# Kernel tuning notes

Measured on AMD Instinct MI355X. Metric: run time of the kernel, lower is better.

## Reference

```python
import math
import jax, jax.numpy as jnp
import numpy as np

HIDDEN = 2048
N_HEAD = 32
N_KV = 8
HEAD_DIM = HIDDEN // N_HEAD  # 64
B, S = 2, 2048


def setup_inputs() -> dict:
    key = jax.random.key(0)
    ks = jax.random.split(key, 9)
    sc_h = 1.0 / math.sqrt(HIDDEN)
    return {
        "X": jax.random.normal(ks[0], (B, S, HIDDEN), jnp.float32),
        "Wq": jax.random.normal(ks[1], (HIDDEN, HIDDEN), jnp.float32) * sc_h,
        "bq": jax.random.normal(ks[2], (HIDDEN,), jnp.float32) * 0.01,
        "Wk": jax.random.normal(ks[3], (N_KV * HEAD_DIM, HIDDEN), jnp.float32) * sc_h,
        "bk": jax.random.normal(ks[4], (N_KV * HEAD_DIM,), jnp.float32) * 0.01,
        "Wv": jax.random.normal(ks[5], (N_KV * HEAD_DIM, HIDDEN), jnp.float32) * sc_h,
        "bv": jax.random.normal(ks[6], (N_KV * HEAD_DIM,), jnp.float32) * 0.01,
        "Wo": jax.random.normal(ks[7], (HIDDEN, HIDDEN), jnp.float32) * sc_h,
        "bo": jax.random.normal(ks[8], (HIDDEN,), jnp.float32) * 0.01,
    }


def reference(X, Wq, bq, Wk, bk, Wv, bv, Wo, bo):
    b, s, _ = X.shape
    g = N_HEAD // N_KV  # query heads per kv head (repeat_interleave group)
    scale = 1.0 / math.sqrt(HEAD_DIM)

    q = X @ Wq.T + bq                       # [B,S,H*D]
    k = X @ Wk.T + bk                       # [B,S,KV*D]
    v = X @ Wv.T + bv                       # [B,S,KV*D]

    # q grouped as (B, KV, g, S, D): head h = kv*g + j matches repeat_interleave on dim=1
    q = q.reshape(b, s, N_KV, g, HEAD_DIM).transpose(0, 2, 3, 1, 4)  # [B,KV,g,S,D]
    k = k.reshape(b, s, N_KV, HEAD_DIM).transpose(0, 2, 1, 3)         # [B,KV,S,D]
    v = v.reshape(b, s, N_KV, HEAD_DIM).transpose(0, 2, 1, 3)         # [B,KV,S,D]

    # scores without materializing repeated K/V: broadcast kv head over g query heads
    scores = jnp.einsum("bkgqd,bkld->bkgql", q, k) * scale            # [B,KV,g,S,S]
    weights = jax.nn.softmax(scores, axis=-1)
    out = jnp.einsum("bkgql,bkld->bkgqd", weights, v)                 # [B,KV,g,S,D]

    # replicate torch's contiguous .view(B, seq, -1) applied to the [B,H,S,D]
    # tensor WITHOUT transposing back: plain row-major reshape of (B,H,S,D).
    out = out.reshape(b, s, N_HEAD * HEAD_DIM)
    return out @ Wo.T + bo
```

## Files before the change

kernel.cpp:

```cpp
#include <hip/hip_runtime.h>

#define HIDDEN 2048
#define NHEADS 32
#define NKV    8
#define HDIM   64
#define BATCH  2
#define SEQ    2048
#define MROWS  (BATCH*SEQ)
#define NQKV   3072

#define SCALEQ 0.18033688011112042f

typedef _Float16 half8_t __attribute__((ext_vector_type(8)));
typedef _Float16 half4_t __attribute__((ext_vector_type(4)));
typedef __fp16   fp16x2_t __attribute__((ext_vector_type(2)));
typedef float    f32x4_t __attribute__((ext_vector_type(4)));

#define AS1 __attribute__((address_space(1)))
#define AS3 __attribute__((address_space(3)))

__device__ __forceinline__ void async_copy16(void* lds, const void* g) {
    __builtin_amdgcn_global_load_lds((AS1 void*)g, (AS3 void*)lds, 16, 0, 0);
}

#define PRIO1 __builtin_amdgcn_s_setprio(1)
#define PRIO0 __builtin_amdgcn_s_setprio(0)
#define BAR   __builtin_amdgcn_s_barrier()


#define STG_A(bi, u, kb) \
    async_copy16(&As[bi][(u)*4096 + ldst], Ag + (size_t)((u)*64) * K + (kb))
#define STG_B(bi, u, kb) \
    async_copy16(&Bs[bi][(u)*4096 + ldst], Bg + (size_t)((u)*64) * K + (kb))

#define LDA2(dst, bi, mh) do {                                                 \
    _Pragma("unroll") for (int mi = 0; mi < 2; ++mi) {                         \
        dst[mi][0] = *(const half8_t*)(&As[bi][abase + ((mh)*2+mi)*1024 + g0]);\
        dst[mi][1] = *(const half8_t*)(&As[bi][abase + ((mh)*2+mi)*1024 + g1]);\
    } } while (0)

#define LDB4(dst, bi) do {                                                     \
    _Pragma("unroll") for (int ni = 0; ni < 4; ++ni) {                         \
        dst[ni][0] = *(const half8_t*)(&Bs[bi][bbase + ni*1024 + g0]);         \
        dst[ni][1] = *(const half8_t*)(&Bs[bi][bbase + ni*1024 + g1]);         \
    } } while (0)

#define MFMA_H(av, mh) do {                                                    \
    _Pragma("unroll") for (int mi = 0; mi < 2; ++mi)                           \
    _Pragma("unroll") for (int ni = 0; ni < 4; ++ni) {                         \
        f32x4_t& cc = acc[(mh)*2 + mi][ni];                                    \
        cc = __builtin_amdgcn_mfma_f32_16x16x32_f16(av[mi][0], b[ni][0], cc, 0, 0, 0); \
        cc = __builtin_amdgcn_mfma_f32_16x16x32_f16(av[mi][1], b[ni][1], cc, 0, 0, 0); \
    } } while (0)

template <typename OutT, bool QKV>
__global__ __launch_bounds__(512, 2) void gemm128(
    const _Float16* __restrict__ A, const _Float16* __restrict__ Bm,
    const float* __restrict__ bias, OutT* __restrict__ C,
    _Float16* __restrict__ kfb, _Float16* __restrict__ vfb,
    int K, int ldc) {
    __shared__ _Float16 As[2][8192];
    __shared__ _Float16 Bs[2][16384];

    const int tid  = threadIdx.x;
    const int wave = tid >> 6;
    const int lane = tid & 63;
    const int quad = lane >> 4;
    const int l16  = lane & 15;
    const int wr   = wave >> 2;
    const int wc   = wave & 3;

    const int nwg = (int)(gridDim.x * gridDim.y);
    const int lin = (int)(blockIdx.y * gridDim.x + blockIdx.x);
    const int q8  = nwg >> 3;
    const int idx = (lin & 7) * q8 + (lin >> 3);
    const int tx  = idx % (int)gridDim.x;
    const int ty  = idx / (int)gridDim.x;
    const int m0  = ty * 128;
    const int n0  = tx * 256;

    const int srow = tid >> 3;
    const int sg   = ((tid & 7) ^ (srow & 7)) << 3;
    const _Float16* Ag = A  + (size_t)(m0 + srow) * K + sg;
    const _Float16* Bg = Bm + (size_t)(n0 + srow) * K + sg;
    const int ldst = wave * 512;

    const int sk = l16 & 7;
    const int g0 = ((0 + quad) ^ sk) << 3;
    const int g1 = ((4 + quad) ^ sk) << 3;
    const int abase = wr * 4096 + l16 * 64;
    const int bbase = wc * 4096 + l16 * 64;

    f32x4_t acc[4][4] = {};
    const int NT = K >> 6;

    STG_A(0, 0, 0);  STG_A(0, 1, 0);
    STG_B(0, 0, 0);  STG_B(0, 1, 0);  STG_B(0, 2, 0);  STG_B(0, 3, 0);
    STG_B(1, 0, 64); STG_B(1, 1, 64); STG_B(1, 2, 64); STG_B(1, 3, 64);
    asm volatile("s_waitcnt vmcnt(4)" ::: "memory");
    BAR;

    for (int t = 0; t < NT; ++t) {
        const int  cur = t & 1;
        const int  kA  = (t + 1) << 6;
        const int  kB  = (t + 2) << 6;
        const bool sA  = (t + 1 < NT);
        const bool sB  = (t + 2 < NT);
        half8_t aL[2][2], aH[2][2], b[4][2];

        LDA2(aL, cur, 0);
        LDB4(b, cur);
        if (sA) { STG_A(cur ^ 1, 0, kA); STG_A(cur ^ 1, 1, kA); }
        BAR;
        PRIO1; MFMA_H(aL, 0); PRIO0;
        BAR;
        LDA2(aH, cur, 1);
        if (sB) { STG_B(cur, 0, kB); STG_B(cur, 1, kB);
                  STG_B(cur, 2, kB); STG_B(cur, 3, kB); }
        BAR;
        PRIO1; MFMA_H(aH, 1); PRIO0;
        if (sB) { asm volatile("s_waitcnt vmcnt(4)" ::: "memory"); }
        else    { asm volatile("s_waitcnt vmcnt(0)" ::: "memory"); }
        BAR;
    }

    if (QKV && n0 >= 2560) {
#pragma unroll
        for (int ni = 0; ni < 4; ++ni) {
            const int c  = n0 + wc * 64 + ni * 16 + l16;
            const int kd = c - 2560;
            const int kv = kd >> 6, d = kd & 63;
            const int dt = (d >> 4) & 3;
            const float bv = bias[c];
#pragma unroll
            for (int mi = 0; mi < 4; ++mi) {
                const int r0   = m0 + wr * 64 + mi * 16 + quad * 4;
                const int bb   = r0 >> 11;
                const int sblk = (r0 & 2047) >> 6;
                const int nt   = (r0 >> 4) & 3;
                half4_t h;
#pragma unroll
                for (int i = 0; i < 4; ++i) h[i] = (_Float16)(acc[mi][ni][i] + bv);
                *(half4_t*)(vfb + ((size_t)(bb * 8 + kv) * 32 + sblk) * 4096 +
                            ((nt * 4 + dt) * 64 + quad * 16 + (d & 15)) * 4) = h;
            }
        }
    } else if (QKV && n0 >= 2048) {
#pragma unroll
        for (int ni = 0; ni < 4; ++ni) {
            const int c  = n0 + wc * 64 + ni * 16 + l16;
            const int kd = c - 2048;
            const int kv = kd >> 6, d = kd & 63;
            const float bv = bias[c];
#pragma unroll
            for (int mi = 0; mi < 4; ++mi) {
                const int r0   = m0 + wr * 64 + mi * 16 + quad * 4;
                const int bb   = r0 >> 11;
                const int sblk = (r0 & 2047) >> 6;
                const int nt   = (r0 >> 4) & 3;
                _Float16* dst = kfb + ((size_t)(bb * 8 + kv) * 32 + sblk) * 4096 +
                    ((nt * 2 + (d >> 5)) * 64 + ((d >> 3) & 3) * 16 + quad * 4) * 8 +
                    (d & 7);
#pragma unroll
                for (int i = 0; i < 4; ++i)
                    dst[i * 8] = (_Float16)(acc[mi][ni][i] + bv);
            }
        }
    } else {
#pragma unroll
        for (int ni = 0; ni < 4; ++ni) {
            const int c  = n0 + wc * 64 + ni * 16 + l16;
            const float bv = bias[c];
#pragma unroll
            for (int mi = 0; mi < 4; ++mi) {
                const int r0 = m0 + wr * 64 + mi * 16 + quad * 4;
#pragma unroll
                for (int i = 0; i < 4; ++i)
                    C[(size_t)(r0 + i) * ldc + c] = (OutT)(acc[mi][ni][i] + bv);
            }
        }
    }
}

__global__ __launch_bounds__(512, 4) void attn_kernel(
    const _Float16* __restrict__ Qb, const _Float16* __restrict__ Kf,
    const _Float16* __restrict__ Vf, _Float16* __restrict__ ctx) {
    __shared__ _Float16 S[16384];

    const int tid  = threadIdx.x;
    const int wave = tid >> 6;
    const int lane = tid & 63;
    const int quad = lane >> 4;
    const int l16  = lane & 15;
    const int qs   = wave >> 2;
    const int wh   = wave & 3;
    const int qt  = blockIdx.x;
    const int bkv = blockIdx.y;
    const int b   = bkv >> 3;
    const int kv  = bkv & 7;
    const int h   = kv * 4 + wh;

    half8_t qa[2][2];
#pragma unroll
    for (int g = 0; g < 2; ++g) {
        const _Float16* qp = Qb +
            ((size_t)(b * SEQ + qt * 64 + qs * 32 + g * 16 + l16)) * HIDDEN +
            h * 64 + quad * 8;
        qa[g][0] = *(const half8_t*)qp;
        qa[g][1] = *(const half8_t*)(qp + 32);
    }

    f32x4_t ot[2][4] = {};
    f32x4_t lacc[2] = {};
    const half4_t ones = {(_Float16)1.f, (_Float16)1.f, (_Float16)1.f, (_Float16)1.f};

    const size_t kvbase = (size_t)(b * 8 + kv) * 32 * 4096;
    const int sh = wave * 512 + lane * 8;

    async_copy16(&S[wave * 512],        Kf + kvbase + sh);
    async_copy16(&S[8192 + wave * 512], Vf + kvbase + sh);

    for (int kt = 0; kt < SEQ / 64; ++kt) {
        __syncthreads();
        const int cur = kt & 1;
        if (kt + 1 < SEQ / 64) {
            const size_t off = kvbase + (size_t)(kt + 1) * 4096 + sh;
            async_copy16(&S[(cur ^ 1) * 4096 + wave * 512],        Kf + off);
            async_copy16(&S[8192 + (cur ^ 1) * 4096 + wave * 512], Vf + off);
        }
        const int kb = cur * 4096, vb = 8192 + cur * 4096;

#pragma unroll
        for (int nt = 0; nt < 4; ++nt) {
            const half8_t kf0 = *(const half8_t*)(&S[kb + ((nt * 2 + 0) * 64 + lane) * 8]);
            const half8_t kf1 = *(const half8_t*)(&S[kb + ((nt * 2 + 1) * 64 + lane) * 8]);
            half4_t p[2];
#pragma unroll
            for (int g = 0; g < 2; ++g) {
                f32x4_t s = {};
                s = __builtin_amdgcn_mfma_f32_16x16x32_f16(kf0, qa[g][0], s, 0, 0, 0);
                s = __builtin_amdgcn_mfma_f32_16x16x32_f16(kf1, qa[g][1], s, 0, 0, 0);
                const fp16x2_t lo = __builtin_amdgcn_cvt_pkrtz(
                    __builtin_amdgcn_exp2f(s[0]), __builtin_amdgcn_exp2f(s[1]));
                const fp16x2_t hi = __builtin_amdgcn_cvt_pkrtz(
                    __builtin_amdgcn_exp2f(s[2]), __builtin_amdgcn_exp2f(s[3]));
                half4_t pv;
                pv[0] = (_Float16)lo[0]; pv[1] = (_Float16)lo[1];
                pv[2] = (_Float16)hi[0]; pv[3] = (_Float16)hi[1];
                p[g] = pv;
                lacc[g] = __builtin_amdgcn_mfma_f32_16x16x16f16(ones, pv, lacc[g], 0, 0, 0);
            }
#pragma unroll
            for (int dt = 0; dt < 4; ++dt) {
                const half4_t vf = *(const half4_t*)(&S[vb + ((nt * 4 + dt) * 64 + lane) * 4]);
                ot[0][dt] = __builtin_amdgcn_mfma_f32_16x16x16f16(vf, p[0], ot[0][dt], 0, 0, 0);
                ot[1][dt] = __builtin_amdgcn_mfma_f32_16x16x16f16(vf, p[1], ot[1][dt], 0, 0, 0);
            }
        }
    }

    __syncthreads();
    _Float16* T = S + wave * 1152;
#pragma unroll
    for (int g = 0; g < 2; ++g) {
        const float inv = 1.f / lacc[g][0];
#pragma unroll
        for (int dt = 0; dt < 4; ++dt) {
            half4_t hh;
#pragma unroll
            for (int r = 0; r < 4; ++r) hh[r] = (_Float16)(ot[g][dt][r] * inv);
            *(half4_t*)(T + l16 * 72 + dt * 16 + quad * 4) = hh;
        }
        __builtin_amdgcn_s_waitcnt(0);
        _Float16* cp = ctx +
            (((size_t)b * 32 + h) * SEQ + qt * 64 + qs * 32 + g * 16 + l16) * 64;
#pragma unroll
        for (int pass = 0; pass < 2; ++pass) {
            const half8_t row = *(const half8_t*)(T + l16 * 72 + pass * 32 + quad * 8);
            *(half8_t*)(cp + pass * 32 + quad * 8) = row;
        }
        __builtin_amdgcn_s_waitcnt(0);
    }
}

__device__ __forceinline__ void cast4(const float* __restrict__ s,
                                      _Float16* __restrict__ d, int i, float sc) {
    const f32x4_t v = ((const f32x4_t*)s)[i];
    half4_t h;
#pragma unroll
    for (int j = 0; j < 4; ++j) h[j] = (_Float16)(v[j] * sc);
    ((half4_t*)d)[i] = h;
}

__global__ __launch_bounds__(256) void prep(
    const float* __restrict__ X,  const float* __restrict__ Wq,
    const float* __restrict__ Wk, const float* __restrict__ Wv,
    const float* __restrict__ Wo, const float* __restrict__ bq,
    const float* __restrict__ bk, const float* __restrict__ bv,
    _Float16* __restrict__ Xh, _Float16* __restrict__ Wqkv,
    _Float16* __restrict__ Woh, float* __restrict__ bqkv) {
    const int bid = blockIdx.x, tid = threadIdx.x;
    if (bid < 8192)       cast4(X,  Xh,   bid * 256 + tid, 1.f);
    else if (bid < 12288) cast4(Wq, Wqkv, (bid - 8192) * 256 + tid, SCALEQ);
    else if (bid < 13312) cast4(Wk, Wqkv + (size_t)HIDDEN * HIDDEN, (bid - 12288) * 256 + tid, 1.f);
    else if (bid < 14336) cast4(Wv, Wqkv + (size_t)(HIDDEN + 512) * HIDDEN, (bid - 13312) * 256 + tid, 1.f);
    else if (bid < 18432) cast4(Wo, Woh,  (bid - 14336) * 256 + tid, 1.f);
    else {
        const int i = (bid - 18432) * 256 + tid;
        if (i < 2048)      bqkv[i] = bq[i] * SCALEQ;
        else if (i < 2560) bqkv[i] = bk[i - 2048];
        else if (i < 3072) bqkv[i] = bv[i - 2560];
    }
}

extern "C" void kernel_launch(void* const* d_in, const int* in_sizes, int n_in,
                              void* d_out, int out_size, void* d_ws, size_t ws_size,
                              hipStream_t stream) {
    const float* X  = (const float*)d_in[0];
    const float* Wq = (const float*)d_in[1];
    const float* bq = (const float*)d_in[2];
    const float* Wk = (const float*)d_in[3];
    const float* bk = (const float*)d_in[4];
    const float* Wv = (const float*)d_in[5];
    const float* bv = (const float*)d_in[6];
    const float* Wo = (const float*)d_in[7];
    const float* bo = (const float*)d_in[8];
    float* out = (float*)d_out;

    char* p = (char*)d_ws;
    _Float16* Xh   = (_Float16*)p; p += (size_t)MROWS * HIDDEN * 2;
    _Float16* Wqkv = (_Float16*)p; p += (size_t)NQKV * HIDDEN * 2;
    _Float16* Woh  = (_Float16*)p; p += (size_t)HIDDEN * HIDDEN * 2;
    float*    bqkv = (float*)p;    p += (size_t)NQKV * 4;
    _Float16* Qb   = (_Float16*)p; p += (size_t)MROWS * HIDDEN * 2;
    _Float16* Kfb  = (_Float16*)p; p += (size_t)16 * 32 * 4096 * 2;
    _Float16* Vfb  = (_Float16*)p; p += (size_t)16 * 32 * 4096 * 2;
    _Float16* ctx  = Xh;

    prep<<<18444, 256, 0, stream>>>(X, Wq, Wk, Wv, Wo, bq, bk, bv,
                                    Xh, Wqkv, Woh, bqkv);

    gemm128<_Float16, true><<<dim3(NQKV / 256, MROWS / 128), 512, 0, stream>>>(
        Xh, Wqkv, bqkv, Qb, Kfb, Vfb, HIDDEN, HIDDEN);

    attn_kernel<<<dim3(SEQ / 64, BATCH * NKV), 512, 0, stream>>>(Qb, Kfb, Vfb, ctx);

    gemm128<float, false><<<dim3(HIDDEN / 256, MROWS / 128), 512, 0, stream>>>(
        ctx, Woh, bo, out, nullptr, nullptr, HIDDEN, HIDDEN);
}
```

Before: 320.9 us.

## Split GEMM into QKV/out kernels, retile QKV to 192 cols, deepen attention pipeline

The templated GEMM is split into a QKV kernel with 128x192 tiles, smaller LDS and launch bounds raised to four blocks per CU, and an output-projection kernel with constant K. The V fragment layout is changed so attention reads half8 vectors. Attention now prefetches two K/V tiles per barrier through a four-slot LDS ring, and computes the softmax row sum with scalar adds plus shuffles instead of an extra MFMA against a ones vector. MFMA sections are wrapped in setprio. The larger attention LDS footprint may reduce occupancy, and register pressure at four QKV blocks per CU may cause spills.

```diff
diff --git a/kernel.cpp b/kernel.cpp
--- a/kernel.cpp
+++ b/kernel.cpp
@@ -28,39 +28,17 @@
 #define BAR   __builtin_amdgcn_s_barrier()
 
 
-#define STG_A(bi, u, kb) \
-    async_copy16(&As[bi][(u)*4096 + ldst], Ag + (size_t)((u)*64) * K + (kb))
-#define STG_B(bi, u, kb) \
-    async_copy16(&Bs[bi][(u)*4096 + ldst], Bg + (size_t)((u)*64) * K + (kb))
-
-#define LDA2(dst, bi, mh) do {                                                 \
-    _Pragma("unroll") for (int mi = 0; mi < 2; ++mi) {                         \
-        dst[mi][0] = *(const half8_t*)(&As[bi][abase + ((mh)*2+mi)*1024 + g0]);\
-        dst[mi][1] = *(const half8_t*)(&As[bi][abase + ((mh)*2+mi)*1024 + g1]);\
-    } } while (0)
-
-#define LDB4(dst, bi) do {                                                     \
-    _Pragma("unroll") for (int ni = 0; ni < 4; ++ni) {                         \
-        dst[ni][0] = *(const half8_t*)(&Bs[bi][bbase + ni*1024 + g0]);         \
-        dst[ni][1] = *(const half8_t*)(&Bs[bi][bbase + ni*1024 + g1]);         \
-    } } while (0)
-
-#define MFMA_H(av, mh) do {                                                    \
-    _Pragma("unroll") for (int mi = 0; mi < 2; ++mi)                           \
-    _Pragma("unroll") for (int ni = 0; ni < 4; ++ni) {                         \
-        f32x4_t& cc = acc[(mh)*2 + mi][ni];                                    \
-        cc = __builtin_amdgcn_mfma_f32_16x16x32_f16(av[mi][0], b[ni][0], cc, 0, 0, 0); \
-        cc = __builtin_amdgcn_mfma_f32_16x16x32_f16(av[mi][1], b[ni][1], cc, 0, 0, 0); \
-    } } while (0)
-
-template <typename OutT, bool QKV>
-__global__ __launch_bounds__(512, 2) void gemm128(
+#define QSTG_A(bi, u, kb) \
+    async_copy16(&As[bi][(u)*4096 + ldst], Ag + (size_t)((u)*64) * 2048 + (kb))
+#define QSTG_B(bi, u, kb) \
+    async_copy16(&Bs[bi][(u)*4096 + ldst], Bg + (size_t)((u)*64) * 2048 + (kb))
+
+__global__ __launch_bounds__(512, 4) void gemm_qkv(
     const _Float16* __restrict__ A, const _Float16* __restrict__ Bm,
-    const float* __restrict__ bias, OutT* __restrict__ C,
-    _Float16* __restrict__ kfb, _Float16* __restrict__ vfb,
-    int K, int ldc) {
+    const float* __restrict__ bias, _Float16* __restrict__ Qb,
+    _Float16* __restrict__ kfb, _Float16* __restrict__ vfb) {
     __shared__ _Float16 As[2][8192];
-    __shared__ _Float16 Bs[2][16384];
+    __shared__ _Float16 Bs[2][12288];
 
     const int tid  = threadIdx.x;
     const int wave = tid >> 6;
@@ -70,68 +48,115 @@
     const int wr   = wave >> 2;
     const int wc   = wave & 3;
 
-    const int nwg = (int)(gridDim.x * gridDim.y);
     const int lin = (int)(blockIdx.y * gridDim.x + blockIdx.x);
-    const int q8  = nwg >> 3;
-    const int idx = (lin & 7) * q8 + (lin >> 3);
-    const int tx  = idx % (int)gridDim.x;
-    const int ty  = idx / (int)gridDim.x;
-    const int m0  = ty * 128;
-    const int n0  = tx * 256;
+    const int idx = (lin & 7) * 64 + (lin >> 3);
+    const int m0  = (idx >> 4) * 128;
+    const int n0  = (idx & 15) * 192;
 
     const int srow = tid >> 3;
     const int sg   = ((tid & 7) ^ (srow & 7)) << 3;
-    const _Float16* Ag = A  + (size_t)(m0 + srow) * K + sg;
-    const _Float16* Bg = Bm + (size_t)(n0 + srow) * K + sg;
+    const _Float16* Ag = A  + (size_t)(m0 + srow) * 2048 + sg;
+    const _Float16* Bg = Bm + (size_t)(n0 + srow) * 2048 + sg;
     const int ldst = wave * 512;
 
     const int sk = l16 & 7;
     const int g0 = ((0 + quad) ^ sk) << 3;
     const int g1 = ((4 + quad) ^ sk) << 3;
     const int abase = wr * 4096 + l16 * 64;
-    const int bbase = wc * 4096 + l16 * 64;
-
-    f32x4_t acc[4][4] = {};
-    const int NT = K >> 6;
-
-    STG_A(0, 0, 0);  STG_A(0, 1, 0);
-    STG_B(0, 0, 0);  STG_B(0, 1, 0);  STG_B(0, 2, 0);  STG_B(0, 3, 0);
-    STG_B(1, 0, 64); STG_B(1, 1, 64); STG_B(1, 2, 64); STG_B(1, 3, 64);
-    asm volatile("s_waitcnt vmcnt(4)" ::: "memory");
+    const int bbase = wc * 3072 + l16 * 64;
+
+    f32x4_t acc[4][3] = {};
+
+    QSTG_A(0, 0, 0);  QSTG_A(0, 1, 0);
+    QSTG_B(0, 0, 0);  QSTG_B(0, 1, 0);  QSTG_B(0, 2, 0);
+    QSTG_B(1, 0, 64); QSTG_B(1, 1, 64); QSTG_B(1, 2, 64);
+    asm volatile("s_waitcnt vmcnt(3)" ::: "memory");
     BAR;
 
-    for (int t = 0; t < NT; ++t) {
+    for (int t = 0; t < 32; ++t) {
         const int  cur = t & 1;
         const int  kA  = (t + 1) << 6;
         const int  kB  = (t + 2) << 6;
-        const bool sA  = (t + 1 < NT);
-        const bool sB  = (t + 2 < NT);
-        half8_t aL[2][2], aH[2][2], b[4][2];
-
-        LDA2(aL, cur, 0);
-        LDB4(b, cur);
-        if (sA) { STG_A(cur ^ 1, 0, kA); STG_A(cur ^ 1, 1, kA); }
-        BAR;
-        PRIO1; MFMA_H(aL, 0); PRIO0;
-        BAR;
-        LDA2(aH, cur, 1);
-        if (sB) { STG_B(cur, 0, kB); STG_B(cur, 1, kB);
-                  STG_B(cur, 2, kB); STG_B(cur, 3, kB); }
-        BAR;
-        PRIO1; MFMA_H(aH, 1); PRIO0;
-        if (sB) { asm volatile("s_waitcnt vmcnt(4)" ::: "memory"); }
+        const bool sA  = (t + 1 < 32);
+        const bool sB  = (t + 2 < 32);
+        half8_t a[2][2], b[3][2];
+
+#pragma unroll
+        for (int mi = 0; mi < 2; ++mi) {
+            a[mi][0] = *(const half8_t*)(&As[cur][abase + mi * 1024 + g0]);
+            a[mi][1] = *(const half8_t*)(&As[cur][abase + mi * 1024 + g1]);
+        }
+#pragma unroll
+        for (int ni = 0; ni < 3; ++ni) {
+            b[ni][0] = *(const half8_t*)(&Bs[cur][bbase + ni * 1024 + g0]);
+            b[ni][1] = *(const half8_t*)(&Bs[cur][bbase + ni * 1024 + g1]);
+        }
+        if (sA) { QSTG_A(cur ^ 1, 0, kA); QSTG_A(cur ^ 1, 1, kA); }
+        BAR;
+        PRIO1;
+#pragma unroll
+        for (int mi = 0; mi < 2; ++mi)
+#pragma unroll
+            for (int ni = 0; ni < 3; ++ni) {
+                acc[mi][ni] = __builtin_amdgcn_mfma_f32_16x16x32_f16(a[mi][0], b[ni][0], acc[mi][ni], 0, 0, 0);
+                acc[mi][ni] = __builtin_amdgcn_mfma_f32_16x16x32_f16(a[mi][1], b[ni][1], acc[mi][ni], 0, 0, 0);
+            }
+        PRIO0;
+        BAR;
+#pragma unroll
+        for (int mi = 0; mi < 2; ++mi) {
+            a[mi][0] = *(const half8_t*)(&As[cur][abase + (2 + mi) * 1024 + g0]);
+            a[mi][1] = *(const half8_t*)(&As[cur][abase + (2 + mi) * 1024 + g1]);
+        }
+        if (sB) { QSTG_B(cur, 0, kB); QSTG_B(cur, 1, kB); QSTG_B(cur, 2, kB); }
+        BAR;
+        PRIO1;
+#pragma unroll
+        for (int mi = 0; mi < 2; ++mi)
+#pragma unroll
+            for (int ni = 0; ni < 3; ++ni) {
+                acc[2 + mi][ni] = __builtin_amdgcn_mfma_f32_16x16x32_f16(a[mi][0], b[ni][0], acc[2 + mi][ni], 0, 0, 0);
+                acc[2 + mi][ni] = __builtin_amdgcn_mfma_f32_16x16x32_f16(a[mi][1], b[ni][1], acc[2 + mi][ni], 0, 0, 0);
+            }
+        PRIO0;
+        if (sB) { asm volatile("s_waitcnt vmcnt(3)" ::: "memory"); }
         else    { asm volatile("s_waitcnt vmcnt(0)" ::: "memory"); }
         BAR;
     }
 
-    if (QKV && n0 >= 2560) {
-#pragma unroll
-        for (int ni = 0; ni < 4; ++ni) {
-            const int c  = n0 + wc * 64 + ni * 16 + l16;
+#pragma unroll
+    for (int ni = 0; ni < 3; ++ni) {
+        const int cbase = n0 + wc * 48 + ni * 16;
+        const int c  = cbase + l16;
+        const float bv = bias[c];
+        if (cbase < 2048) {
+#pragma unroll
+            for (int mi = 0; mi < 4; ++mi) {
+                const int r0 = m0 + wr * 64 + mi * 16 + quad * 4;
+#pragma unroll
+                for (int i = 0; i < 4; ++i)
+                    Qb[(size_t)(r0 + i) * HIDDEN + c] = (_Float16)(acc[mi][ni][i] + bv);
+            }
+        } else if (cbase < 2560) {
+            const int kd = c - 2048;
+            const int kvh = kd >> 6, d = kd & 63;
+#pragma unroll
+            for (int mi = 0; mi < 4; ++mi) {
+                const int r0   = m0 + wr * 64 + mi * 16 + quad * 4;
+                const int bb   = r0 >> 11;
+                const int sblk = (r0 & 2047) >> 6;
+                const int nt   = (r0 >> 4) & 3;
+                _Float16* dst = kfb + ((size_t)(bb * 8 + kvh) * 32 + sblk) * 4096 +
+                    ((nt * 2 + (d >> 5)) * 64 + ((d >> 3) & 3) * 16 + quad * 4) * 8 +
+                    (d & 7);
+#pragma unroll
+                for (int i = 0; i < 4; ++i)
+                    dst[i * 8] = (_Float16)(acc[mi][ni][i] + bv);
+            }
+        } else {
             const int kd = c - 2560;
-            const int kv = kd >> 6, d = kd & 63;
+            const int kvh = kd >> 6, d = kd & 63;
             const int dt = (d >> 4) & 3;
-            const float bv = bias[c];
 #pragma unroll
             for (int mi = 0; mi < 4; ++mi) {
                 const int r0   = m0 + wr * 64 + mi * 16 + quad * 4;
@@ -141,43 +166,120 @@
                 half4_t h;
 #pragma unroll
                 for (int i = 0; i < 4; ++i) h[i] = (_Float16)(acc[mi][ni][i] + bv);
-                *(half4_t*)(vfb + ((size_t)(bb * 8 + kv) * 32 + sblk) * 4096 +
-                            ((nt * 4 + dt) * 64 + quad * 16 + (d & 15)) * 4) = h;
-            }
-        }
-    } else if (QKV && n0 >= 2048) {
+                *(half4_t*)(vfb + ((size_t)(bb * 8 + kvh) * 32 + sblk) * 4096 +
+                            (nt * 2 + (dt >> 1)) * 512 + quad * 128 +
+                            (d & 15) * 8 + (dt & 1) * 4) = h;
+            }
+        }
+    }
+}
+
+#define OSTG_A(bi, u, kb) \
+    async_copy16(&As[bi][(u)*4096 + ldst], Ag + (size_t)((u)*64) * 2048 + (kb))
+#define OSTG_B(bi, u, kb) \
+    async_copy16(&Bs[bi][(u)*4096 + ldst], Bg + (size_t)((u)*64) * 2048 + (kb))
+
+__global__ __launch_bounds__(512, 2) void gemm_out(
+    const _Float16* __restrict__ A, const _Float16* __restrict__ Bm,
+    const float* __restrict__ bias, float* __restrict__ C) {
+    __shared__ _Float16 As[2][8192];
+    __shared__ _Float16 Bs[2][16384];
+
+    const int tid  = threadIdx.x;
+    const int wave = tid >> 6;
+    const int lane = tid & 63;
+    const int quad = lane >> 4;
+    const int l16  = lane & 15;
+    const int wr   = wave >> 2;
+    const int wc   = wave & 3;
+
+    const int lin = (int)(blockIdx.y * gridDim.x + blockIdx.x);
+    const int idx = (lin & 7) * 32 + (lin >> 3);
+    const int m0  = (idx >> 3) * 128;
+    const int n0  = (idx & 7) * 256;
+
+    const int srow = tid >> 3;
+    const int sg   = ((tid & 7) ^ (srow & 7)) << 3;
+    const _Float16* Ag = A  + (size_t)(m0 + srow) * 2048 + sg;
+    const _Float16* Bg = Bm + (size_t)(n0 + srow) * 2048 + sg;
+    const int ldst = wave * 512;
+
+    const int sk = l16 & 7;
+    const int g0 = ((0 + quad) ^ sk) << 3;
+    const int g1 = ((4 + quad) ^ sk) << 3;
+    const int abase = wr * 4096 + l16 * 64;
+    const int bbase = wc * 4096 + l16 * 64;
+
+    f32x4_t acc[4][4] = {};
+
+    OSTG_A(0, 0, 0);  OSTG_A(0, 1, 0);
+    OSTG_B(0, 0, 0);  OSTG_B(0, 1, 0);  OSTG_B(0, 2, 0);  OSTG_B(0, 3, 0);
+    OSTG_B(1, 0, 64); OSTG_B(1, 1, 64); OSTG_B(1, 2, 64); OSTG_B(1, 3, 64);
+    asm volatile("s_waitcnt vmcnt(4)" ::: "memory");
+    BAR;
+
+    for (int t = 0; t < 32; ++t) {
+        const int  cur = t & 1;
+        const int  kA  = (t + 1) << 6;
+        const int  kB  = (t + 2) << 6;
+        const bool sA  = (t + 1 < 32);
+        const bool sB  = (t + 2 < 32);
+        half8_t a[2][2], b[4][2];
+
+#pragma unroll
+        for (int mi = 0; mi < 2; ++mi) {
+            a[mi][0] = *(const half8_t*)(&As[cur][abase + mi * 1024 + g0]);
+            a[mi][1] = *(const half8_t*)(&As[cur][abase + mi * 1024 + g1]);
+        }
 #pragma unroll
         for (int ni = 0; ni < 4; ++ni) {
-            const int c  = n0 + wc * 64 + ni * 16 + l16;
-            const int kd = c - 2048;
-            const int kv = kd >> 6, d = kd & 63;
-            const float bv = bias[c];
-#pragma unroll
-            for (int mi = 0; mi < 4; ++mi) {
-                const int r0   = m0 + wr * 64 + mi * 16 + quad * 4;
-                const int bb   = r0 >> 11;
-                const int sblk = (r0 & 2047) >> 6;
-                const int nt   = (r0 >> 4) & 3;
-                _Float16* dst = kfb + ((size_t)(bb * 8 + kv) * 32 + sblk) * 4096 +
-                    ((nt * 2 + (d >> 5)) * 64 + ((d >> 3) & 3) * 16 + quad * 4) * 8 +
-                    (d & 7);
-#pragma unroll
-                for (int i = 0; i < 4; ++i)
-                    dst[i * 8] = (_Float16)(acc[mi][ni][i] + bv);
-            }
-        }
-    } else {
-#pragma unroll
-        for (int ni = 0; ni < 4; ++ni) {
-            const int c  = n0 + wc * 64 + ni * 16 + l16;
-            const float bv = bias[c];
-#pragma unroll
-            for (int mi = 0; mi < 4; ++mi) {
-                const int r0 = m0 + wr * 64 + mi * 16 + quad * 4;
-#pragma unroll
-                for (int i = 0; i < 4; ++i)
-                    C[(size_t)(r0 + i) * ldc + c] = (OutT)(acc[mi][ni][i] + bv);
-            }
+            b[ni][0] = *(const half8_t*)(&Bs[cur][bbase + ni * 1024 + g0]);
+            b[ni][1] = *(const half8_t*)(&Bs[cur][bbase + ni * 1024 + g1]);
+        }
+        if (sA) { OSTG_A(cur ^ 1, 0, kA); OSTG_A(cur ^ 1, 1, kA); }
+        BAR;
+        PRIO1;
+#pragma unroll
+        for (int mi = 0; mi < 2; ++mi)
+#pragma unroll
+            for (int ni = 0; ni < 4; ++ni) {
+                acc[mi][ni] = __builtin_amdgcn_mfma_f32_16x16x32_f16(a[mi][0], b[ni][0], acc[mi][ni], 0, 0, 0);
+                acc[mi][ni] = __builtin_amdgcn_mfma_f32_16x16x32_f16(a[mi][1], b[ni][1], acc[mi][ni], 0, 0, 0);
+            }
+        PRIO0;
+        BAR;
+#pragma unroll
+        for (int mi = 0; mi < 2; ++mi) {
+            a[mi][0] = *(const half8_t*)(&As[cur][abase + (2 + mi) * 1024 + g0]);
+            a[mi][1] = *(const half8_t*)(&As[cur][abase + (2 + mi) * 1024 + g1]);
+        }
+        if (sB) { OSTG_B(cur, 0, kB); OSTG_B(cur, 1, kB);
+                  OSTG_B(cur, 2, kB); OSTG_B(cur, 3, kB); }
+        BAR;
+        PRIO1;
+#pragma unroll
+        for (int mi = 0; mi < 2; ++mi)
+#pragma unroll
+            for (int ni = 0; ni < 4; ++ni) {
+                acc[2 + mi][ni] = __builtin_amdgcn_mfma_f32_16x16x32_f16(a[mi][0], b[ni][0], acc[2 + mi][ni], 0, 0, 0);
+                acc[2 + mi][ni] = __builtin_amdgcn_mfma_f32_16x16x32_f16(a[mi][1], b[ni][1], acc[2 + mi][ni], 0, 0, 0);
+            }
+        PRIO0;
+        if (sB) { asm volatile("s_waitcnt vmcnt(4)" ::: "memory"); }
+        else    { asm volatile("s_waitcnt vmcnt(0)" ::: "memory"); }
+        BAR;
+    }
+
+#pragma unroll
+    for (int ni = 0; ni < 4; ++ni) {
+        const int c = n0 + wc * 64 + ni * 16 + l16;
+        const float bv = bias[c];
+#pragma unroll
+        for (int mi = 0; mi < 4; ++mi) {
+            const int r0 = m0 + wr * 64 + mi * 16 + quad * 4;
+#pragma unroll
+            for (int i = 0; i < 4; ++i)
+                C[(size_t)(r0 + i) * HIDDEN + c] = acc[mi][ni][i] + bv;
         }
     }
 }
@@ -185,7 +287,7 @@
 __global__ __launch_bounds__(512, 4) void attn_kernel(
     const _Float16* __restrict__ Qb, const _Float16* __restrict__ Kf,
     const _Float16* __restrict__ Vf, _Float16* __restrict__ ctx) {
-    __shared__ _Float16 S[16384];
+    __shared__ _Float16 S[32768];
 
     const int tid  = threadIdx.x;
     const int wave = tid >> 6;
@@ -211,59 +313,84 @@
     }
 
     f32x4_t ot[2][4] = {};
-    f32x4_t lacc[2] = {};
-    const half4_t ones = {(_Float16)1.f, (_Float16)1.f, (_Float16)1.f, (_Float16)1.f};
+    float fl[2] = {0.f, 0.f};
 
     const size_t kvbase = (size_t)(b * 8 + kv) * 32 * 4096;
     const int sh = wave * 512 + lane * 8;
 
-    async_copy16(&S[wave * 512],        Kf + kvbase + sh);
-    async_copy16(&S[8192 + wave * 512], Vf + kvbase + sh);
-
-    for (int kt = 0; kt < SEQ / 64; ++kt) {
+#pragma unroll
+    for (int t = 0; t < 2; ++t) {
+        async_copy16(&S[t * 4096 + wave * 512],         Kf + kvbase + (size_t)t * 4096 + sh);
+        async_copy16(&S[16384 + t * 4096 + wave * 512], Vf + kvbase + (size_t)t * 4096 + sh);
+    }
+
+    for (int j = 0; j < 16; ++j) {
         __syncthreads();
-        const int cur = kt & 1;
-        if (kt + 1 < SEQ / 64) {
-            const size_t off = kvbase + (size_t)(kt + 1) * 4096 + sh;
-            async_copy16(&S[(cur ^ 1) * 4096 + wave * 512],        Kf + off);
-            async_copy16(&S[8192 + (cur ^ 1) * 4096 + wave * 512], Vf + off);
-        }
-        const int kb = cur * 4096, vb = 8192 + cur * 4096;
-
-#pragma unroll
-        for (int nt = 0; nt < 4; ++nt) {
-            const half8_t kf0 = *(const half8_t*)(&S[kb + ((nt * 2 + 0) * 64 + lane) * 8]);
-            const half8_t kf1 = *(const half8_t*)(&S[kb + ((nt * 2 + 1) * 64 + lane) * 8]);
-            half4_t p[2];
-#pragma unroll
-            for (int g = 0; g < 2; ++g) {
-                f32x4_t s = {};
-                s = __builtin_amdgcn_mfma_f32_16x16x32_f16(kf0, qa[g][0], s, 0, 0, 0);
-                s = __builtin_amdgcn_mfma_f32_16x16x32_f16(kf1, qa[g][1], s, 0, 0, 0);
-                const fp16x2_t lo = __builtin_amdgcn_cvt_pkrtz(
-                    __builtin_amdgcn_exp2f(s[0]), __builtin_amdgcn_exp2f(s[1]));
-                const fp16x2_t hi = __builtin_amdgcn_cvt_pkrtz(
-                    __builtin_amdgcn_exp2f(s[2]), __builtin_amdgcn_exp2f(s[3]));
-                half4_t pv;
-                pv[0] = (_Float16)lo[0]; pv[1] = (_Float16)lo[1];
-                pv[2] = (_Float16)hi[0]; pv[3] = (_Float16)hi[1];
-                p[g] = pv;
-                lacc[g] = __builtin_amdgcn_mfma_f32_16x16x16f16(ones, pv, lacc[g], 0, 0, 0);
-            }
-#pragma unroll
-            for (int dt = 0; dt < 4; ++dt) {
-                const half4_t vf = *(const half4_t*)(&S[vb + ((nt * 4 + dt) * 64 + lane) * 4]);
-                ot[0][dt] = __builtin_amdgcn_mfma_f32_16x16x16f16(vf, p[0], ot[0][dt], 0, 0, 0);
-                ot[1][dt] = __builtin_amdgcn_mfma_f32_16x16x16f16(vf, p[1], ot[1][dt], 0, 0, 0);
-            }
-        }
+        if (j < 15) {
+#pragma unroll
+            for (int t = 0; t < 2; ++t) {
+                const int tile = 2 * j + 2 + t;
+                const int slot = tile & 3;
+                const size_t off = kvbase + (size_t)tile * 4096 + sh;
+                async_copy16(&S[slot * 4096 + wave * 512],         Kf + off);
+                async_copy16(&S[16384 + slot * 4096 + wave * 512], Vf + off);
+            }
+        }
+#pragma unroll
+        for (int tt = 0; tt < 2; ++tt) {
+            const int slot = (2 * j + tt) & 3;
+            const int kb = slot * 4096, vb = 16384 + slot * 4096;
+#pragma unroll
+            for (int nt = 0; nt < 4; ++nt) {
+                const half8_t kf0 = *(const half8_t*)(&S[kb + ((nt * 2 + 0) * 64 + lane) * 8]);
+                const half8_t kf1 = *(const half8_t*)(&S[kb + ((nt * 2 + 1) * 64 + lane) * 8]);
+                half4_t p[2];
+#pragma unroll
+                for (int g = 0; g < 2; ++g) {
+                    f32x4_t s = {};
+                    PRIO1;
+                    s = __builtin_amdgcn_mfma_f32_16x16x32_f16(kf0, qa[g][0], s, 0, 0, 0);
+                    s = __builtin_amdgcn_mfma_f32_16x16x32_f16(kf1, qa[g][1], s, 0, 0, 0);
+                    PRIO0;
+                    const float e0 = __builtin_amdgcn_exp2f(s[0]);
+                    const float e1 = __builtin_amdgcn_exp2f(s[1]);
+                    const float e2 = __builtin_amdgcn_exp2f(s[2]);
+                    const float e3 = __builtin_amdgcn_exp2f(s[3]);
+                    fl[g] += (e0 + e1) + (e2 + e3);
+                    const fp16x2_t lo = __builtin_amdgcn_cvt_pkrtz(e0, e1);
+                    const fp16x2_t hi = __builtin_amdgcn_cvt_pkrtz(e2, e3);
+                    half4_t pv;
+                    pv[0] = (_Float16)lo[0]; pv[1] = (_Float16)lo[1];
+                    pv[2] = (_Float16)hi[0]; pv[3] = (_Float16)hi[1];
+                    p[g] = pv;
+                }
+#pragma unroll
+                for (int dp = 0; dp < 2; ++dp) {
+                    const half8_t vv = *(const half8_t*)(&S[vb + ((nt * 2 + dp) * 64 + lane) * 8]);
+                    const half4_t vlo = {vv[0], vv[1], vv[2], vv[3]};
+                    const half4_t vhi = {vv[4], vv[5], vv[6], vv[7]};
+                    PRIO1;
+                    ot[0][dp * 2]     = __builtin_amdgcn_mfma_f32_16x16x16f16(vlo, p[0], ot[0][dp * 2], 0, 0, 0);
+                    ot[1][dp * 2]     = __builtin_amdgcn_mfma_f32_16x16x16f16(vlo, p[1], ot[1][dp * 2], 0, 0, 0);
+                    ot[0][dp * 2 + 1] = __builtin_amdgcn_mfma_f32_16x16x16f16(vhi, p[0], ot[0][dp * 2 + 1], 0, 0, 0);
+                    ot[1][dp * 2 + 1] = __builtin_amdgcn_mfma_f32_16x16x16f16(vhi, p[1], ot[1][dp * 2 + 1], 0, 0, 0);
+                    PRIO0;
+                }
+            }
+        }
+    }
+
+#pragma unroll
+    for (int g = 0; g < 2; ++g) {
+        fl[g] += __shfl_xor(fl[g], 16);
+        fl[g] += __shfl_xor(fl[g], 32);
     }
 
     __syncthreads();
     _Float16* T = S + wave * 1152;
 #pragma unroll
     for (int g = 0; g < 2; ++g) {
-        const float inv = 1.f / lacc[g][0];
+        const float inv = 1.f / fl[g];
 #pragma unroll
         for (int dt = 0; dt < 4; ++dt) {
             half4_t hh;
@@ -340,11 +467,11 @@
     prep<<<18444, 256, 0, stream>>>(X, Wq, Wk, Wv, Wo, bq, bk, bv,
                                     Xh, Wqkv, Woh, bqkv);
 
-    gemm128<_Float16, true><<<dim3(NQKV / 256, MROWS / 128), 512, 0, stream>>>(
-        Xh, Wqkv, bqkv, Qb, Kfb, Vfb, HIDDEN, HIDDEN);
+    gemm_qkv<<<dim3(NQKV / 192, MROWS / 128), 512, 0, stream>>>(
+        Xh, Wqkv, bqkv, Qb, Kfb, Vfb);
 
     attn_kernel<<<dim3(SEQ / 64, BATCH * NKV), 512, 0, stream>>>(Qb, Kfb, Vfb, ctx);
 
-    gemm128<float, false><<<dim3(HIDDEN / 256, MROWS / 128), 512, 0, stream>>>(
-        ctx, Woh, bo, out, nullptr, nullptr, HIDDEN, HIDDEN);
-}
+    gemm_out<<<dim3(HIDDEN / 256, MROWS / 128), 512, 0, stream>>>(
+        ctx, Woh, bo, out);
+}
```

After: 311.5 us. 1.03x faster.
